# Optimization experiments

Hardware: AMD Instinct MI355X
Metric: run time of the kernel (lower is better)

## Reference

```python
import jax, jax.numpy as jnp
import numpy as np

DIM = 128
NUM_LAYERS = 2
FF_MULT = 4
RADIUS = 0.2
K = 8
B, N, L = 8, 2048, 4096
NEG = -1e30


def setup_inputs() -> dict:
    key = jax.random.key(0)
    ks = jax.random.split(key, 12)
    C = DIM
    s = 1.0 / np.sqrt(C)
    w = lambda k, shape, sc: jax.random.normal(k, shape, dtype=jnp.float32) * sc
    inp = {
        "q_xyz": jax.random.uniform(ks[0], (B, N, 3), dtype=jnp.float32),
        "q_feat": jax.random.normal(ks[1], (B, N, C), dtype=jnp.float32),
        "kv_xyz": jax.random.uniform(ks[2], (B, L, 3), dtype=jnp.float32),
        "kv_feat": jax.random.normal(ks[3], (B, L, C), dtype=jnp.float32),
        "kv_pad": jnp.zeros((B, L), dtype=bool),
        # PointTransformerConv params (stacked over layers)
        "W_lin": w(ks[4], (NUM_LAYERS, C, C), s),   # value projection (with bias)
        "b_lin": jnp.zeros((NUM_LAYERS, C), jnp.float32),
        "W_src": w(ks[5], (NUM_LAYERS, C, C), s),   # lin_src, no bias
        "W_dst": w(ks[6], (NUM_LAYERS, C, C), s),   # lin_dst, no bias
        "W_attn": w(ks[7], (NUM_LAYERS, C, C), s),  # attn_nn = Linear+ReLU
        "b_attn": jnp.zeros((NUM_LAYERS, C), jnp.float32),
        "ln1_g": jnp.ones((NUM_LAYERS, C), jnp.float32),
        "ln1_b": jnp.zeros((NUM_LAYERS, C), jnp.float32),
        "W_ff1": w(ks[8], (NUM_LAYERS, C, FF_MULT * C), s),
        "b_ff1": jnp.zeros((NUM_LAYERS, FF_MULT * C), jnp.float32),
        "W_ff2": w(ks[9], (NUM_LAYERS, FF_MULT * C, C), 1.0 / np.sqrt(FF_MULT * C)),
        "b_ff2": jnp.zeros((NUM_LAYERS, C), jnp.float32),
        "ln2_g": jnp.ones((NUM_LAYERS, C), jnp.float32),
        "ln2_b": jnp.zeros((NUM_LAYERS, C), jnp.float32),
    }
    return inp


def _layernorm(x, g, b):
    mu = x.mean(-1, keepdims=True)
    var = ((x - mu) ** 2).mean(-1, keepdims=True)
    return (x - mu) * jax.lax.rsqrt(var + 1e-5) * g + b


def _gather(feats, idx):
    # feats: [B, L, C], idx: [B, N, K] -> [B, N, K, C]
    b, n, k = idx.shape
    g = jnp.take_along_axis(feats, idx.reshape(b, n * k)[:, :, None], axis=1)
    return g.reshape(b, n, k, feats.shape[-1])


def _forward(q_xyz, q_feat, kv_xyz, kv_feat, kv_pad,
             W_lin, b_lin, W_src, W_dst, W_attn, b_attn,
             ln1_g, ln1_b, W_ff1, b_ff1, W_ff2, b_ff2, ln2_g, ln2_b):
    # radius neighbor search (per-batch, fixed K neighbors with validity mask)
    d2 = jnp.sum((q_xyz[:, :, None, :] - kv_xyz[:, None, :, :]) ** 2, axis=-1)  # [B,N,L]
    valid_pair = (d2 <= RADIUS * RADIUS) & (~kv_pad)[:, None, :]
    negd = jnp.where(valid_pair, -d2, NEG)
    negv, idx = jax.lax.top_k(negd, K)          # [B,N,K] nearest-in-ball
    evalid = negv > 0.5 * NEG                   # edge validity mask [B,N,K]

    out = q_feat
    for i in range(NUM_LAYERS):
        # PointTransformerConv, pos_nn = ZeroPos => delta = 0
        aj = _gather(kv_feat @ W_src[i], idx)                    # [B,N,K,C]
        vj = _gather(kv_feat @ W_lin[i] + b_lin[i], idx)         # [B,N,K,C]
        ai = out @ W_dst[i]                                      # [B,N,C]
        logits = jax.nn.relu((ai[:, :, None, :] - aj) @ W_attn[i] + b_attn[i])
        logits = jnp.where(evalid[..., None], logits, NEG)
        m = logits.max(axis=2, keepdims=True)
        e = jnp.exp(logits - m) * evalid[..., None]
        attn = e / jnp.maximum(e.sum(axis=2, keepdims=True), 1e-9)  # per-channel softmax over neighbors
        upd = jnp.sum(attn * vj, axis=2)                         # [B,N,C] scatter-add over edges
        out = _layernorm(out + upd, ln1_g[i], ln1_b[i])
        h = jax.nn.gelu(out @ W_ff1[i] + b_ff1[i], approximate=False)
        out = _layernorm(out + h @ W_ff2[i] + b_ff2[i], ln2_g[i], ln2_b[i])
    return out


def reference(q_xyz, q_feat, kv_xyz, kv_feat, kv_pad,
              W_lin, b_lin, W_src, W_dst, W_attn, b_attn,
              ln1_g, ln1_b, W_ff1, b_ff1, W_ff2, b_ff2, ln2_g, ln2_b):
    return _forward(q_xyz, q_feat, kv_xyz, kv_feat, kv_pad,
                    W_lin, b_lin, W_src, W_dst, W_attn, b_attn,
                    ln1_g, ln1_b, W_ff1, b_ff1, W_ff2, b_ff2, ln2_g, ln2_b)
```

## Files before the change

kernel.cpp:

```cpp
#include <hip/hip_runtime.h>
#include <hip/hip_bf16.h>
#include <math.h>

#define DIM 128
#define BB 8
#define NN 2048
#define LL 4096
#define KK 8

typedef __hip_bfloat16 bf16;
typedef unsigned long long ull;
typedef __attribute__((ext_vector_type(8))) short short8;
typedef __attribute__((ext_vector_type(4))) float float4v;

__device__ __forceinline__ float toF(float x){ return x; }
__device__ __forceinline__ float toF(bf16 x){ return __bfloat162float(x); }
__device__ __forceinline__ void st(float* p, float v){ *p = v; }
__device__ __forceinline__ void st(bf16*  p, float v){ *p = __float2bfloat16(v); }
__device__ __forceinline__ unsigned short f2bf(float f){
  union { bf16 b; unsigned short u; } cv; cv.b = __float2bfloat16(f); return cv.u;
}
__device__ __forceinline__ float2 ld2bf(const bf16* p){
  const unsigned u = *(const unsigned*)p;
  return make_float2(__uint_as_float(u << 16), __uint_as_float(u & 0xFFFF0000u));
}
__device__ __forceinline__ void st2bf(bf16* p, float a, float b){
  *(unsigned*)p = (unsigned)f2bf(a) | ((unsigned)f2bf(b) << 16);
}

__device__ __forceinline__ float gelu_exact(float x){
  return 0.5f * x * (1.0f + erff(x * 0.70710678118654752f));
}

__device__ __forceinline__ float waveSum64(float v){
  #pragma unroll
  for (int o = 32; o > 0; o >>= 1) v += __shfl_xor(v, o, 64);
  return v;
}
__device__ __forceinline__ float quadSum16(float v){
  #pragma unroll
  for (int o = 8; o > 0; o >>= 1) v += __shfl_xor(v, o, 64);
  return v;
}

__device__ __forceinline__ void topk_insert_u(ull (&m)[KK], ull key){
  m[KK-1] = key;
  #pragma unroll
  for (int t = KK-1; t > 0; --t){
    if (m[t] < m[t-1]){ ull tmp = m[t]; m[t] = m[t-1]; m[t-1] = tmp; }
  }
}

#define NC3 125
__device__ __forceinline__ void packOne(const float* __restrict__ src,
                                        bf16* __restrict__ dst, int idx, int nshift){
  const int k = idx >> nshift;
  const int n = idx & ((1 << nshift) - 1);
  const int N = 1 << nshift;
  st(&dst[((size_t)(k>>3)*N + n)*8 + (k&7)], src[idx]);
}

__global__ __launch_bounds__(1024) void setup_all(const float* __restrict__ kv_xyz,
                                                  const float* __restrict__ q_xyz,
                                                  float4* __restrict__ bpts,
                                                  int* __restrict__ offs,
                                                  int* __restrict__ qsrt,
                                                  const float* __restrict__ Wlin,
                                                  const float* __restrict__ Wff1,
                                                  const float* __restrict__ Wff2,
                                                  const float* __restrict__ Wsrc,
                                                  const float* __restrict__ Wdst,
                                                  const float* __restrict__ Wattn,
                                                  bf16* __restrict__ WlinP,
                                                  bf16* __restrict__ Wff1P,
                                                  bf16* __restrict__ Wff2P,
                                                  bf16* __restrict__ WsaP,
                                                  bf16* __restrict__ WdaP)
{
  __shared__ int cnt[NC3];
  __shared__ int off[NC3+1];
  __shared__ float row[8][DIM];
  const int bid = blockIdx.x;
  const int tid = threadIdx.x;
  if (bid < 16){
    const int b   = bid & 7;
    const int role= bid >> 3;
    if (tid < NC3) cnt[tid] = 0;
    __syncthreads();
    if (role == 0){
      const float* kvp = kv_xyz + (size_t)b * LL * 3;
      float px[4], py[4], pz[4]; int pc[4];
      #pragma unroll
      for (int i = 0; i < 4; i++){
        const int e = tid + i*1024;
        px[i] = kvp[3*e]; py[i] = kvp[3*e+1]; pz[i] = kvp[3*e+2];
        const int cx = min((int)(px[i]*5.f), 4);
        const int cy = min((int)(py[i]*5.f), 4);
        const int cz = min((int)(pz[i]*5.f), 4);
        pc[i] = (cz*5 + cy)*5 + cx;
        atomicAdd(&cnt[pc[i]], 1);
      }
      __syncthreads();
      if (tid == 0){
        int acc = 0;
        for (int c = 0; c < NC3; c++){ off[c] = acc; acc += cnt[c]; }
        off[NC3] = acc;
      }
      __syncthreads();
      if (tid < NC3) cnt[tid] = 0;
      __syncthreads();
      float4* dst = bpts + (size_t)b * LL;
      #pragma unroll
      for (int i = 0; i < 4; i++){
        const int e = tid + i*1024;
        const int pos = off[pc[i]] + atomicAdd(&cnt[pc[i]], 1);
        dst[pos] = make_float4(px[i], py[i], pz[i], __int_as_float(e));
      }
      if (tid < NC3 + 1) offs[b*126 + tid] = off[tid];
    } else {
      const float* qp = q_xyz + (size_t)b * NN * 3;
      int pc[2];
      #pragma unroll
      for (int i = 0; i < 2; i++){
        const int e = tid + i*1024;
        const float x = qp[3*e], y = qp[3*e+1], z = qp[3*e+2];
        const int cx = min((int)(x*5.f), 4);
        const int cy = min((int)(y*5.f), 4);
        const int cz = min((int)(z*5.f), 4);
        pc[i] = (cz*5 + cy)*5 + cx;
        atomicAdd(&cnt[pc[i]], 1);
      }
      __syncthreads();
      if (tid == 0){
        int acc = 0;
        for (int c = 0; c < NC3; c++){ off[c] = acc; acc += cnt[c]; }
        off[NC3] = acc;
      }
      __syncthreads();
      if (tid < NC3) cnt[tid] = 0;
      __syncthreads();
      int* dst = qsrt + (size_t)b * NN;
      #pragma unroll
      for (int i = 0; i < 2; i++){
        const int e = tid + i*1024;
        const int pos = off[pc[i]] + atomicAdd(&cnt[pc[i]], 1);
        dst[pos] = e;
      }
    }
  } else if (bid < 304){
    int i = (bid - 16)*1024 + tid;
    if (i < 32768){
      const int l = i >> 14, r = i & 16383;
      packOne(Wlin + (size_t)l*16384, WlinP + (size_t)l*16384, r, 7);
    } else if (i < 163840){
      i -= 32768;
      const int l = i >> 16, r = i & 65535;
      packOne(Wff1 + (size_t)l*65536, Wff1P + (size_t)l*65536, r, 9);
    } else {
      i -= 163840;
      const int l = i >> 16, r = i & 65535;
      packOne(Wff2 + (size_t)l*65536, Wff2P + (size_t)l*65536, r, 7);
    }
  } else {
    const int grp = tid >> 7;
    const int c = tid & 127;
    const int tt = (bid - 304)*8 + grp;
    const int r = tt & 127, which = (tt >> 7) & 1, lay = tt >> 8;
    const float* Wx = (which ? Wdst : Wsrc) + (size_t)lay*DIM*DIM;
    const float* Wa = Wattn + (size_t)lay*DIM*DIM;
    row[grp][c] = Wx[r*DIM + c];
    __syncthreads();
    float acc = 0.f;
    for (int j = 0; j < DIM; j++) acc = fmaf(row[grp][j], Wa[j*DIM + c], acc);
    bf16* dst = (which ? WdaP : WsaP) + (size_t)lay*DIM*DIM;
    st(&dst[((size_t)(r>>3)*DIM + c)*8 + (r&7)], acc);
  }
}

#define QBLK 8
#define SPL 32
__global__ __launch_bounds__(256) void knn_query(const float* __restrict__ q_xyz,
                                                 const float4* __restrict__ bpts,
                                                 const int* __restrict__ offs,
                                                 const int* __restrict__ qsrt,
                                                 int* __restrict__ idx)
{
  __shared__ ull cd[QBLK*257];
  const int tid  = threadIdx.x;
  const int s    = tid & 31;
  const int qloc = tid >> 5;
  const int b    = blockIdx.y;
  const int qbase = blockIdx.x * QBLK;
  const int qid = qsrt[b*NN + qbase + qloc];
  const size_t qo = ((size_t)b * NN + qid) * 3;
  const float qx = q_xyz[qo], qy = q_xyz[qo+1], qz = q_xyz[qo+2];
  const ull THRKEY = ((ull)0x3D23D70Bu << 32);
  ull kthr = THRKEY;
  ull m[KK];
  #pragma unroll
  for (int k = 0; k < KK; k++) m[k] = ~0ULL;
  const int qcx = min((int)(qx*5.f), 4);
  const int qcy = min((int)(qy*5.f), 4);
  const int qcz = min((int)(qz*5.f), 4);
  const int* ofb = offs + b*126;
  const float4* bp = bpts + (size_t)b * LL;
  const int cx0 = max(qcx-1, 0), cx1 = min(qcx+1, 4);
  int st9[9], en9[9];
  float4 hd[9];
  #pragma unroll
  for (int u = 0; u < 9; u++){
    const int dz = u/3 - 1, dy = u%3 - 1;
    const int cz = qcz + dz, cy = qcy + dy;
    const bool ok = (cz >= 0) & (cz <= 4) & (cy >= 0) & (cy <= 4);
    const int rowc = (cz*5 + cy)*5;
    int a0 = 0, e0 = 0;
    if (ok){ a0 = ofb[rowc + cx0] + s; e0 = ofb[rowc + cx1 + 1]; }
    st9[u] = a0; en9[u] = e0;
    const int pa = (a0 < e0) ? a0 : 0;
    hd[u] = bp[pa];
  }
  #pragma unroll
  for (int u = 0; u < 9; u++){
    int p = st9[u];
    const int e = en9[u];
    if (p < e){
      float4 pt = hd[u];
      while (true){
        const int pn = p + SPL;
        const bool hn = pn < e;
        float4 nx;
        if (hn) nx = bp[pn];
        const float dx = qx - pt.x, dy = qy - pt.y, dz = qz - pt.z;
        const float d2 = dx*dx + dy*dy + dz*dz;
        const ull key = ((ull)__float_as_uint(d2) << 32) | (unsigned)__float_as_int(pt.w);
        if (key < kthr){
          topk_insert_u(m, key);
          kthr = (m[KK-1] < THRKEY) ? m[KK-1] : THRKEY;
        }
        if (!hn) break;
        pt = nx; p = pn;
      }
    }
  }
  #pragma unroll
  for (int k = 0; k < KK; k++) cd[qloc*257 + k*32 + s] = m[k];
  __syncthreads();
  if (tid < 64){
    const int q = tid >> 3, g = tid & 7;
    ull mm[KK];
    #pragma unroll
    for (int k = 0; k < KK; k++) mm[k] = ~0ULL;
    #pragma unroll
    for (int u = 0; u < 4; u++){
      const int sl = g + 8*u;
      #pragma unroll
      for (int k = 0; k < KK; k++){
        const ull key = cd[q*257 + k*32 + sl];
        if (key < mm[KK-1]) topk_insert_u(mm, key);
      }
    }
    #pragma unroll
    for (int k = 0; k < KK; k++) cd[q*257 + k*32 + g] = mm[k];
    if (tid < QBLK){
      ull f[KK];
      #pragma unroll
      for (int k = 0; k < KK; k++) f[k] = ~0ULL;
      #pragma unroll
      for (int k = 0; k < 8; k++)
        for (int g2 = 0; g2 < 8; g2++){
          const ull key = cd[tid*257 + k*32 + g2];
          if (key < f[KK-1]) topk_insert_u(f, key);
        }
      const int oq = b * NN + qsrt[b*NN + qbase + tid];
      #pragma unroll
      for (int k = 0; k < KK; k++) idx[oq*KK + k] = (int)(unsigned)(f[k] & 0xFFFFFFFFu);
    }
  }
}

__device__ __forceinline__ void stage_A_f32(const float* __restrict__ A, size_t r0,
                                            int kd, int kc, unsigned short* As, int tid){
  #pragma unroll
  for (int i = 0; i < 8; i++){
    const int f = tid + i*256;
    const int row = f >> 5, c4 = (f & 31) * 4;
    const float4 v = *(const float4*)&A[(r0+row)*kd + kc + c4];
    uint2 u;
    u.x = (unsigned)f2bf(v.x) | ((unsigned)f2bf(v.y) << 16);
    u.y = (unsigned)f2bf(v.z) | ((unsigned)f2bf(v.w) << 16);
    *(uint2*)&As[row*136 + c4] = u;
  }
}
__device__ __forceinline__ void stage_A_bf16(const bf16* __restrict__ A, size_t r0,
                                             int kd, int kc, unsigned short* As, int tid){
  #pragma unroll
  for (int i = 0; i < 8; i++){
    const int f = tid + i*256;
    const int row = f >> 5, c4 = (f & 31) * 4;
    *(uint2*)&As[row*136 + c4] = *(const uint2*)&A[(r0+row)*kd + kc + c4];
  }
}

__global__ __launch_bounds__(256) void gemm_all(const float* __restrict__ kvf,
                                                const float* __restrict__ q_feat,
                                                const bf16* __restrict__ WsaP,
                                                const bf16* __restrict__ WlinP,
                                                const bf16* __restrict__ WdaP0,
                                                const float* __restrict__ b_lin,
                                                bf16* __restrict__ srcA0,
                                                bf16* __restrict__ linp0,
                                                bf16* __restrict__ srcA1,
                                                bf16* __restrict__ linp1,
                                                bf16* __restrict__ qA)
{
  __shared__ __align__(16) unsigned short As[64*136];
  const int bid = blockIdx.x;
  const int tid = threadIdx.x;
  const int wid = tid >> 6, ln = tid & 63, qd = ln >> 4, cl = ln & 15;
  if (bid < 1024){
    const int lay = bid >> 9;
    const size_t r0 = (size_t)(bid & 511) * 64;
    const bf16* Wp0 = WsaP  + (size_t)lay * DIM * DIM;
    const bf16* Wp1 = WlinP + (size_t)lay * DIM * DIM;
    const float* bias1 = b_lin + lay * DIM;
    bf16* Y0 = lay ? srcA1 : srcA0;
    bf16* Y1 = lay ? linp1 : linp0;
    stage_A_f32(kvf, r0, 128, 0, As, tid);
    __syncthreads();
    float4v ac0[8], ac1[8];
    #pragma unroll
    for (int t = 0; t < 8; t++){ ac0[t] = (float4v){0.f,0.f,0.f,0.f}; ac1[t] = (float4v){0.f,0.f,0.f,0.f}; }
    #pragma unroll
    for (int ks = 0; ks < 4; ks++){
      const short8 a = *(const short8*)&As[(wid*16 + cl)*136 + (ks*4 + qd)*8];
      const size_t wo = (size_t)(ks*4 + qd)*DIM + cl;
      const short8* wb0 = (const short8*)Wp0 + wo;
      const short8* wb1 = (const short8*)Wp1 + wo;
      #pragma unroll
      for (int t = 0; t < 8; t++){
        const short8 b0 = wb0[t*16];
        ac0[t] = __builtin_amdgcn_mfma_f32_16x16x32_bf16(a, b0, ac0[t], 0, 0, 0);
        const short8 b1 = wb1[t*16];
        ac1[t] = __builtin_amdgcn_mfma_f32_16x16x32_bf16(a, b1, ac1[t], 0, 0, 0);
      }
    }
    #pragma unroll
    for (int t = 0; t < 8; t++){
      const int col = t*16 + cl;
      const float bv = bias1[col];
      #pragma unroll
      for (int r = 0; r < 4; r++){
        const size_t row = r0 + wid*16 + qd*4 + r;
        st(&Y0[row*DIM + col], ac0[t][r]);
        st(&Y1[row*DIM + col], ac1[t][r] + bv);
      }
    }
  } else {
    const size_t r0 = (size_t)(bid - 1024) * 64;
    stage_A_f32(q_feat, r0, 128, 0, As, tid);
    __syncthreads();
    float4v acc[8];
    #pragma unroll
    for (int t = 0; t < 8; t++) acc[t] = (float4v){0.f,0.f,0.f,0.f};
    #pragma unroll
    for (int ks = 0; ks < 4; ks++){
      const short8 a = *(const short8*)&As[(wid*16 + cl)*136 + (ks*4 + qd)*8];
      const short8* wb = (const short8*)WdaP0 + (size_t)(ks*4 + qd)*DIM + cl;
      #pragma unroll
      for (int t = 0; t < 8; t++){
        const short8 b = wb[t*16];
        acc[t] = __builtin_amdgcn_mfma_f32_16x16x32_bf16(a, b, acc[t], 0, 0, 0);
      }
    }
    #pragma unroll
    for (int t = 0; t < 8; t++){
      const int col = t*16 + cl;
      #pragma unroll
      for (int r = 0; r < 4; r++){
        const size_t row = r0 + wid*16 + qd*4 + r;
        st(&qA[row*DIM + col], acc[t][r]);
      }
    }
  }
}

__global__ __launch_bounds__(256) void mfma_ff1(const bf16* __restrict__ A,
                                                const bf16* __restrict__ Wp,
                                                const float* __restrict__ bias,
                                                bf16* __restrict__ Y)
{
  __shared__ __align__(16) unsigned short As[64*136];
  const int tid = threadIdx.x;
  const size_t r0 = (size_t)blockIdx.x * 64;
  const int nblk = blockIdx.y * 128;
  stage_A_bf16(A, r0, 128, 0, As, tid);
  __syncthreads();
  const int wid = tid >> 6, ln = tid & 63, qd = ln >> 4, cl = ln & 15;
  float4v acc[8];
  #pragma unroll
  for (int t = 0; t < 8; t++) acc[t] = (float4v){0.f,0.f,0.f,0.f};
  #pragma unroll
  for (int ks = 0; ks < 4; ks++){
    const short8 a = *(const short8*)&As[(wid*16 + cl)*136 + (ks*4 + qd)*8];
    const short8* wb = (const short8*)Wp + (size_t)(ks*4 + qd)*512 + nblk + cl;
    #pragma unroll
    for (int t = 0; t < 8; t++){
      const short8 b = wb[t*16];
      acc[t] = __builtin_amdgcn_mfma_f32_16x16x32_bf16(a, b, acc[t], 0, 0, 0);
    }
  }
  #pragma unroll
  for (int t = 0; t < 8; t++){
    const int col = nblk + t*16 + cl;
    const float bv = bias[col];
    #pragma unroll
    for (int r = 0; r < 4; r++){
      const size_t row = r0 + wid*16 + qd*4 + r;
      st(&Y[row*512 + col], gelu_exact(acc[t][r] + bv));
    }
  }
}

template<bool EMITQA>
__global__ __launch_bounds__(256) void mfma_ff2ln(const bf16* __restrict__ A,
                                                  const bf16* __restrict__ Wp,
                                                  const float* __restrict__ b2,
                                                  const bf16* __restrict__ resid,
                                                  const float* __restrict__ g,
                                                  const float* __restrict__ bb,
                                                  float* __restrict__ Y,
                                                  const bf16* __restrict__ WqP,
                                                  bf16* __restrict__ qA)
{
  __shared__ __align__(16) unsigned short As[64*136];
  const int tid = threadIdx.x;
  const size_t r0 = (size_t)blockIdx.x * 64;
  const int wid = tid >> 6, ln = tid & 63, qd = ln >> 4, cl = ln & 15;
  float4v acc[8];
  #pragma unroll
  for (int t = 0; t < 8; t++) acc[t] = (float4v){0.f,0.f,0.f,0.f};
  for (int kc = 0; kc < 512; kc += 128){
    __syncthreads();
    stage_A_bf16(A, r0, 512, kc, As, tid);
    __syncthreads();
    const int k8c = kc >> 3;
    #pragma unroll
    for (int ks = 0; ks < 4; ks++){
      const short8 a = *(const short8*)&As[(wid*16 + cl)*136 + (ks*4 + qd)*8];
      const short8* wb = (const short8*)Wp + (size_t)(k8c + ks*4 + qd)*DIM + cl;
      #pragma unroll
      for (int t = 0; t < 8; t++){
        const short8 b = wb[t*16];
        acc[t] = __builtin_amdgcn_mfma_f32_16x16x32_bf16(a, b, acc[t], 0, 0, 0);
      }
    }
  }
  float v[8][4];
  #pragma unroll
  for (int t = 0; t < 8; t++){
    const int col = t*16 + cl;
    const float bv = b2[col];
    #pragma unroll
    for (int r = 0; r < 4; r++){
      const size_t row = r0 + wid*16 + qd*4 + r;
      v[t][r] = acc[t][r] + bv + toF(resid[row*DIM + col]);
    }
  }
  #pragma unroll
  for (int r = 0; r < 4; r++){
    float s = 0.f;
    #pragma unroll
    for (int t = 0; t < 8; t++) s += v[t][r];
    const float mu = quadSum16(s) * (1.f/DIM);
    float q = 0.f;
    #pragma unroll
    for (int t = 0; t < 8; t++){ const float d = v[t][r] - mu; q += d*d; }
    const float inv = rsqrtf(quadSum16(q) * (1.f/DIM) + 1e-5f);
    const size_t row = r0 + wid*16 + qd*4 + r;
    #pragma unroll
    for (int t = 0; t < 8; t++){
      const int col = t*16 + cl;
      const float y = (v[t][r] - mu) * inv * g[col] + bb[col];
      v[t][r] = y;
      Y[row*DIM + col] = y;
    }
  }
  if (EMITQA){
    __syncthreads();
    #pragma unroll
    for (int t = 0; t < 8; t++){
      #pragma unroll
      for (int r = 0; r < 4; r++)
        As[(wid*16 + qd*4 + r)*136 + t*16 + cl] = f2bf(v[t][r]);
    }
    float4v qacc[8];
    #pragma unroll
    for (int t = 0; t < 8; t++) qacc[t] = (float4v){0.f,0.f,0.f,0.f};
    #pragma unroll
    for (int ks = 0; ks < 4; ks++){
      const short8 a = *(const short8*)&As[(wid*16 + cl)*136 + (ks*4 + qd)*8];
      const short8* wb = (const short8*)WqP + (size_t)(ks*4 + qd)*DIM + cl;
      #pragma unroll
      for (int t = 0; t < 8; t++){
        const short8 b = wb[t*16];
        qacc[t] = __builtin_amdgcn_mfma_f32_16x16x32_bf16(a, b, qacc[t], 0, 0, 0);
      }
    }
    #pragma unroll
    for (int t = 0; t < 8; t++){
      const int col = t*16 + cl;
      #pragma unroll
      for (int r = 0; r < 4; r++){
        const size_t row = r0 + wid*16 + qd*4 + r;
        st(&qA[row*DIM + col], qacc[t][r]);
      }
    }
  }
}

__global__ __launch_bounds__(256) void attn_ln1(const bf16* __restrict__ qA,
                                                const bf16* __restrict__ srcA,
                                                const bf16* __restrict__ linp,
                                                const int* __restrict__ idx,
                                                const int* __restrict__ qsrt,
                                                const float* __restrict__ b_attn,
                                                const float* __restrict__ feat,
                                                const float* __restrict__ g,
                                                const float* __restrict__ bb,
                                                bf16* __restrict__ out1)
{
  const int tid = threadIdx.x;
  const int wv = tid >> 6, ln = tid & 63;
  const int sp = blockIdx.x * 4 + wv;
  const int b = sp >> 11;
  const int q = b * NN + qsrt[b*NN + (sp & 2047)];
  const bf16* sbase = srcA + (size_t)b * LL * DIM;
  const bf16* vbase = linp + (size_t)b * LL * DIM;
  const int c0 = 2*ln;
  const float2 ba = *(const float2*)&b_attn[c0];
  const float2 qa2 = ld2bf(&qA[(size_t)q*DIM + c0]);
  const float qa0 = qa2.x + ba.x, qa1 = qa2.y + ba.y;
  int ids[KK]; float l0[KK], l1[KK];
  float m0 = -1e30f, m1 = -1e30f;
  #pragma unroll
  for (int k = 0; k < KK; k++){
    const int id = idx[q*KK + k]; ids[k] = id;
    if (id >= 0){
      const float2 s2 = ld2bf(&sbase[(size_t)id*DIM + c0]);
      l0[k] = fmaxf(qa0 - s2.x, 0.f); m0 = fmaxf(m0, l0[k]);
      l1[k] = fmaxf(qa1 - s2.y, 0.f); m1 = fmaxf(m1, l1[k]);
    } else { l0[k] = 0.f; l1[k] = 0.f; }
  }
  float sum0 = 0.f, sum1 = 0.f, upd0 = 0.f, upd1 = 0.f;
  #pragma unroll
  for (int k = 0; k < KK; k++) if (ids[k] >= 0){
    const float e0 = expf(l0[k] - m0); l0[k] = e0; sum0 += e0;
    const float e1 = expf(l1[k] - m1); l1[k] = e1; sum1 += e1;
  }
  if (sum0 > 0.f){
    const float i0 = 1.f / sum0, i1 = 1.f / sum1;
    #pragma unroll
    for (int k = 0; k < KK; k++) if (ids[k] >= 0){
      const float2 v2 = ld2bf(&vbase[(size_t)ids[k]*DIM + c0]);
      upd0 = fmaf(l0[k]*i0, v2.x, upd0);
      upd1 = fmaf(l1[k]*i1, v2.y, upd1);
    }
  }
  const float2 f2 = *(const float2*)&feat[(size_t)q*DIM + c0];
  const float x0 = f2.x + upd0;
  const float x1 = f2.y + upd1;
  const float mu = waveSum64(x0 + x1) * (1.f/DIM);
  const float d0 = x0 - mu, d1 = x1 - mu;
  const float var = waveSum64(d0*d0 + d1*d1) * (1.f/DIM);
  const float inv = rsqrtf(var + 1e-5f);
  const float2 gg = *(const float2*)&g[c0];
  const float2 bbv = *(const float2*)&bb[c0];
  st2bf(&out1[(size_t)q*DIM + c0], d0 * inv * gg.x + bbv.x, d1 * inv * gg.y + bbv.y);
}

extern "C" void kernel_launch(void* const* d_in, const int* in_sizes, int n_in,
                              void* d_out, int out_size, void* d_ws, size_t ws_size,
                              hipStream_t stream)
{
  const float* q_xyz  = (const float*)d_in[0];
  const float* q_feat = (const float*)d_in[1];
  const float* kv_xyz = (const float*)d_in[2];
  const float* kv_feat= (const float*)d_in[3];
  const float* W_lin  = (const float*)d_in[5];
  const float* b_lin  = (const float*)d_in[6];
  const float* W_src  = (const float*)d_in[7];
  const float* W_dst  = (const float*)d_in[8];
  const float* W_attn = (const float*)d_in[9];
  const float* b_attn = (const float*)d_in[10];
  const float* ln1_g  = (const float*)d_in[11];
  const float* ln1_b  = (const float*)d_in[12];
  const float* W_ff1  = (const float*)d_in[13];
  const float* b_ff1  = (const float*)d_in[14];
  const float* W_ff2  = (const float*)d_in[15];
  const float* b_ff2  = (const float*)d_in[16];
  const float* ln2_g  = (const float*)d_in[17];
  const float* ln2_b  = (const float*)d_in[18];
  float* out = (float*)d_out;

  const int MQ  = BB * NN;
  const int MKV = BB * LL;

  char* p = (char*)d_ws;
  int*    idxb  = (int*)p;    p += (size_t)MQ * KK * 4;
  float4* bpts  = (float4*)p; p += (size_t)BB * LL * 16;
  int*    boffs = (int*)p;    p += (size_t)BB * 126 * 4;
  int*    qsrt  = (int*)p;    p += (size_t)BB * NN * 4;
  bf16*  WsaP  = (bf16*)p;  p += (size_t)2 * DIM * DIM * 2;
  bf16*  WdaP  = (bf16*)p;  p += (size_t)2 * DIM * DIM * 2;
  bf16*  WlinP = (bf16*)p;  p += (size_t)2 * DIM * DIM * 2;
  bf16*  Wff1P = (bf16*)p;  p += (size_t)2 * DIM * 4*DIM * 2;
  bf16*  Wff2P = (bf16*)p;  p += (size_t)2 * 4*DIM * DIM * 2;
  float* feat  = (float*)p; p += (size_t)MQ * DIM * 4;
  bf16*  out1  = (bf16*)p;  p += (size_t)MQ * DIM * 2;
  bf16*  srcA0 = (bf16*)p;  p += (size_t)MKV * DIM * 2;
  bf16*  linp0 = (bf16*)p;  p += (size_t)MKV * DIM * 2;
  bf16*  srcA1 = (bf16*)p;  p += (size_t)MKV * DIM * 2;
  bf16*  linp1 = (bf16*)p;  p += (size_t)MKV * DIM * 2;
  bf16*  qA    = (bf16*)p;  p += (size_t)MQ * DIM * 2;
  bf16*  hbuf  = (bf16*)p;  p += (size_t)MQ * 4*DIM * 2;

  setup_all<<<368, 1024, 0, stream>>>(kv_xyz, q_xyz, bpts, boffs, qsrt,
                                      W_lin, W_ff1, W_ff2, W_src, W_dst, W_attn,
                                      WlinP, Wff1P, Wff2P, WsaP, WdaP);
  knn_query<<<dim3(NN/QBLK, BB), 256, 0, stream>>>(q_xyz, bpts, boffs, qsrt, idxb);
  gemm_all<<<1280, 256, 0, stream>>>(kv_feat, q_feat, WsaP, WlinP, WdaP,
                                     b_lin, srcA0, linp0, srcA1, linp1, qA);

  attn_ln1<<<MQ/4, 256, 0, stream>>>(qA, srcA0, linp0, idxb, qsrt, b_attn,
                                     q_feat, ln1_g, ln1_b, out1);
  mfma_ff1<<<dim3(MQ/64, 4), 256, 0, stream>>>(out1, Wff1P, b_ff1, hbuf);
  mfma_ff2ln<true><<<MQ/64, 256, 0, stream>>>(hbuf, Wff2P, b_ff2, out1,
                                              ln2_g, ln2_b, feat,
                                              WdaP + DIM*DIM, qA);
  attn_ln1<<<MQ/4, 256, 0, stream>>>(qA, srcA1, linp1, idxb, qsrt, b_attn + DIM,
                                     feat, ln1_g + DIM, ln1_b + DIM, out1);
  mfma_ff1<<<dim3(MQ/64, 4), 256, 0, stream>>>(out1, Wff1P + DIM*4*DIM,
                                               b_ff1 + 4*DIM, hbuf);
  mfma_ff2ln<false><<<MQ/64, 256, 0, stream>>>(hbuf, Wff2P + 4*DIM*DIM,
                                               b_ff2 + DIM, out1,
                                               ln2_g + DIM, ln2_b + DIM, out,
                                               nullptr, nullptr);
}
```

Measured before the change: 284.8 us.

## Fuse FF1 and FF2+LN into one kernel and overlap weight packing with kNN

Fuses the FF1 GEMM with GELU into the FF2+LayerNorm kernel. Each 128-column hidden chunk is written to per-wave shared memory and consumed right away, so the MQ x 512 hidden buffer no longer round-trips through global memory. The residual is read from the staged shared A tile instead of global. Point binning is split into its own small kernel, and weight packing is interleaved with kNN query blocks in one launch so the packing work overlaps the search. Two launches per layer become one, at the cost of more shared memory per block and less FF1 parallelism, since there is no longer a grid dimension over N-blocks.

```diff
diff --git a/kernel.cpp b/kernel.cpp
--- a/kernel.cpp
+++ b/kernel.cpp
@@ -15,6 +15,9 @@
 
 __device__ __forceinline__ float toF(float x){ return x; }
 __device__ __forceinline__ float toF(bf16 x){ return __bfloat162float(x); }
+__device__ __forceinline__ float bfuToF(unsigned short u){
+  return __uint_as_float((unsigned)u << 16);
+}
 __device__ __forceinline__ void st(float* p, float v){ *p = v; }
 __device__ __forceinline__ void st(bf16*  p, float v){ *p = __float2bfloat16(v); }
 __device__ __forceinline__ unsigned short f2bf(float f){
@@ -52,6 +55,83 @@
 }
 
 #define NC3 125
+__global__ __launch_bounds__(1024) void bin_kernel(const float* __restrict__ kv_xyz,
+                                                   const float* __restrict__ q_xyz,
+                                                   float4* __restrict__ bpts,
+                                                   int* __restrict__ offs,
+                                                   int* __restrict__ qsrt)
+{
+  __shared__ int cnt[NC3];
+  __shared__ int off[NC3+1];
+  const int b   = blockIdx.x & 7;
+  const int role= blockIdx.x >> 3;
+  const int tid = threadIdx.x;
+  if (tid < NC3) cnt[tid] = 0;
+  __syncthreads();
+  if (role == 0){
+    const float* kvp = kv_xyz + (size_t)b * LL * 3;
+    float px[4], py[4], pz[4]; int pc[4];
+    #pragma unroll
+    for (int i = 0; i < 4; i++){
+      const int e = tid + i*1024;
+      px[i] = kvp[3*e]; py[i] = kvp[3*e+1]; pz[i] = kvp[3*e+2];
+      const int cx = min((int)(px[i]*5.f), 4);
+      const int cy = min((int)(py[i]*5.f), 4);
+      const int cz = min((int)(pz[i]*5.f), 4);
+      pc[i] = (cz*5 + cy)*5 + cx;
+      atomicAdd(&cnt[pc[i]], 1);
+    }
+    __syncthreads();
+    if (tid == 0){
+      int acc = 0;
+      for (int c = 0; c < NC3; c++){ off[c] = acc; acc += cnt[c]; }
+      off[NC3] = acc;
+    }
+    __syncthreads();
+    if (tid < NC3) cnt[tid] = 0;
+    __syncthreads();
+    float4* dst = bpts + (size_t)b * LL;
+    #pragma unroll
+    for (int i = 0; i < 4; i++){
+      const int e = tid + i*1024;
+      const int pos = off[pc[i]] + atomicAdd(&cnt[pc[i]], 1);
+      dst[pos] = make_float4(px[i], py[i], pz[i], __int_as_float(e));
+    }
+    if (tid < NC3 + 1) offs[b*126 + tid] = off[tid];
+  } else {
+    const float* qp = q_xyz + (size_t)b * NN * 3;
+    int pc[2];
+    #pragma unroll
+    for (int i = 0; i < 2; i++){
+      const int e = tid + i*1024;
+      const float x = qp[3*e], y = qp[3*e+1], z = qp[3*e+2];
+      const int cx = min((int)(x*5.f), 4);
+      const int cy = min((int)(y*5.f), 4);
+      const int cz = min((int)(z*5.f), 4);
+      pc[i] = (cz*5 + cy)*5 + cx;
+      atomicAdd(&cnt[pc[i]], 1);
+    }
+    __syncthreads();
+    if (tid == 0){
+      int acc = 0;
+      for (int c = 0; c < NC3; c++){ off[c] = acc; acc += cnt[c]; }
+      off[NC3] = acc;
+    }
+    __syncthreads();
+    if (tid < NC3) cnt[tid] = 0;
+    __syncthreads();
+    int* dst = qsrt + (size_t)b * NN;
+    #pragma unroll
+    for (int i = 0; i < 2; i++){
+      const int e = tid + i*1024;
+      const int pos = off[pc[i]] + atomicAdd(&cnt[pc[i]], 1);
+      dst[pos] = e;
+    }
+  }
+}
+
+#define QBLK 8
+#define SPL 32
 __device__ __forceinline__ void packOne(const float* __restrict__ src,
                                         bf16* __restrict__ dst, int idx, int nshift){
   const int k = idx >> nshift;
@@ -60,137 +140,67 @@
   st(&dst[((size_t)(k>>3)*N + n)*8 + (k&7)], src[idx]);
 }
 
-__global__ __launch_bounds__(1024) void setup_all(const float* __restrict__ kv_xyz,
-                                                  const float* __restrict__ q_xyz,
-                                                  float4* __restrict__ bpts,
-                                                  int* __restrict__ offs,
-                                                  int* __restrict__ qsrt,
-                                                  const float* __restrict__ Wlin,
-                                                  const float* __restrict__ Wff1,
-                                                  const float* __restrict__ Wff2,
-                                                  const float* __restrict__ Wsrc,
-                                                  const float* __restrict__ Wdst,
-                                                  const float* __restrict__ Wattn,
-                                                  bf16* __restrict__ WlinP,
-                                                  bf16* __restrict__ Wff1P,
-                                                  bf16* __restrict__ Wff2P,
-                                                  bf16* __restrict__ WsaP,
-                                                  bf16* __restrict__ WdaP)
+__global__ __launch_bounds__(256) void knn_pack(const float* __restrict__ q_xyz,
+                                                const float4* __restrict__ bpts,
+                                                const int* __restrict__ offs,
+                                                const int* __restrict__ qsrt,
+                                                int* __restrict__ idx,
+                                                const float* __restrict__ Wlin,
+                                                const float* __restrict__ Wff1,
+                                                const float* __restrict__ Wff2,
+                                                const float* __restrict__ Wsrc,
+                                                const float* __restrict__ Wdst,
+                                                const float* __restrict__ Wattn,
+                                                bf16* __restrict__ WlinP,
+                                                bf16* __restrict__ Wff1P,
+                                                bf16* __restrict__ Wff2P,
+                                                bf16* __restrict__ WsaP,
+                                                bf16* __restrict__ WdaP)
 {
-  __shared__ int cnt[NC3];
-  __shared__ int off[NC3+1];
-  __shared__ float row[8][DIM];
+  __shared__ __align__(16) unsigned char smem[16448];
   const int bid = blockIdx.x;
   const int tid = threadIdx.x;
-  if (bid < 16){
-    const int b   = bid & 7;
-    const int role= bid >> 3;
-    if (tid < NC3) cnt[tid] = 0;
-    __syncthreads();
-    if (role == 0){
-      const float* kvp = kv_xyz + (size_t)b * LL * 3;
-      float px[4], py[4], pz[4]; int pc[4];
-      #pragma unroll
-      for (int i = 0; i < 4; i++){
-        const int e = tid + i*1024;
-        px[i] = kvp[3*e]; py[i] = kvp[3*e+1]; pz[i] = kvp[3*e+2];
-        const int cx = min((int)(px[i]*5.f), 4);
-        const int cy = min((int)(py[i]*5.f), 4);
-        const int cz = min((int)(pz[i]*5.f), 4);
-        pc[i] = (cz*5 + cy)*5 + cx;
-        atomicAdd(&cnt[pc[i]], 1);
-      }
+  bool isKnn; int rid;
+  if (bid < 2816){ isKnn = !(bid & 1); rid = bid >> 1; }
+  else { isKnn = true; rid = 1408 + (bid - 2816); }
+
+  if (!isKnn){
+    if (rid < 1152){
+      int i = rid*256 + tid;
+      if (i < 32768){
+        const int l = i >> 14, r = i & 16383;
+        packOne(Wlin + (size_t)l*16384, WlinP + (size_t)l*16384, r, 7);
+      } else if (i < 163840){
+        i -= 32768;
+        const int l = i >> 16, r = i & 65535;
+        packOne(Wff1 + (size_t)l*65536, Wff1P + (size_t)l*65536, r, 9);
+      } else {
+        i -= 163840;
+        const int l = i >> 16, r = i & 65535;
+        packOne(Wff2 + (size_t)l*65536, Wff2P + (size_t)l*65536, r, 7);
+      }
+    } else {
+      float* row = (float*)smem;
+      const int half = tid >> 7;
+      const int c = tid & 127;
+      const int tt = (rid - 1152)*2 + half;
+      const int r = tt & 127, which = (tt >> 7) & 1, lay = tt >> 8;
+      const float* Wx = (which ? Wdst : Wsrc) + (size_t)lay*DIM*DIM;
+      const float* Wa = Wattn + (size_t)lay*DIM*DIM;
+      row[half*DIM + c] = Wx[r*DIM + c];
       __syncthreads();
-      if (tid == 0){
-        int acc = 0;
-        for (int c = 0; c < NC3; c++){ off[c] = acc; acc += cnt[c]; }
-        off[NC3] = acc;
-      }
-      __syncthreads();
-      if (tid < NC3) cnt[tid] = 0;
-      __syncthreads();
-      float4* dst = bpts + (size_t)b * LL;
-      #pragma unroll
-      for (int i = 0; i < 4; i++){
-        const int e = tid + i*1024;
-        const int pos = off[pc[i]] + atomicAdd(&cnt[pc[i]], 1);
-        dst[pos] = make_float4(px[i], py[i], pz[i], __int_as_float(e));
-      }
-      if (tid < NC3 + 1) offs[b*126 + tid] = off[tid];
-    } else {
-      const float* qp = q_xyz + (size_t)b * NN * 3;
-      int pc[2];
-      #pragma unroll
-      for (int i = 0; i < 2; i++){
-        const int e = tid + i*1024;
-        const float x = qp[3*e], y = qp[3*e+1], z = qp[3*e+2];
-        const int cx = min((int)(x*5.f), 4);
-        const int cy = min((int)(y*5.f), 4);
-        const int cz = min((int)(z*5.f), 4);
-        pc[i] = (cz*5 + cy)*5 + cx;
-        atomicAdd(&cnt[pc[i]], 1);
-      }
-      __syncthreads();
-      if (tid == 0){
-        int acc = 0;
-        for (int c = 0; c < NC3; c++){ off[c] = acc; acc += cnt[c]; }
-        off[NC3] = acc;
-      }
-      __syncthreads();
-      if (tid < NC3) cnt[tid] = 0;
-      __syncthreads();
-      int* dst = qsrt + (size_t)b * NN;
-      #pragma unroll
-      for (int i = 0; i < 2; i++){
-        const int e = tid + i*1024;
-        const int pos = off[pc[i]] + atomicAdd(&cnt[pc[i]], 1);
-        dst[pos] = e;
-      }
-    }
-  } else if (bid < 304){
-    int i = (bid - 16)*1024 + tid;
-    if (i < 32768){
-      const int l = i >> 14, r = i & 16383;
-      packOne(Wlin + (size_t)l*16384, WlinP + (size_t)l*16384, r, 7);
-    } else if (i < 163840){
-      i -= 32768;
-      const int l = i >> 16, r = i & 65535;
-      packOne(Wff1 + (size_t)l*65536, Wff1P + (size_t)l*65536, r, 9);
-    } else {
-      i -= 163840;
-      const int l = i >> 16, r = i & 65535;
-      packOne(Wff2 + (size_t)l*65536, Wff2P + (size_t)l*65536, r, 7);
-    }
-  } else {
-    const int grp = tid >> 7;
-    const int c = tid & 127;
-    const int tt = (bid - 304)*8 + grp;
-    const int r = tt & 127, which = (tt >> 7) & 1, lay = tt >> 8;
-    const float* Wx = (which ? Wdst : Wsrc) + (size_t)lay*DIM*DIM;
-    const float* Wa = Wattn + (size_t)lay*DIM*DIM;
-    row[grp][c] = Wx[r*DIM + c];
-    __syncthreads();
-    float acc = 0.f;
-    for (int j = 0; j < DIM; j++) acc = fmaf(row[grp][j], Wa[j*DIM + c], acc);
-    bf16* dst = (which ? WdaP : WsaP) + (size_t)lay*DIM*DIM;
-    st(&dst[((size_t)(r>>3)*DIM + c)*8 + (r&7)], acc);
-  }
-}
-
-#define QBLK 8
-#define SPL 32
-__global__ __launch_bounds__(256) void knn_query(const float* __restrict__ q_xyz,
-                                                 const float4* __restrict__ bpts,
-                                                 const int* __restrict__ offs,
-                                                 const int* __restrict__ qsrt,
-                                                 int* __restrict__ idx)
-{
-  __shared__ ull cd[QBLK*257];
-  const int tid  = threadIdx.x;
+      float acc = 0.f;
+      for (int j = 0; j < DIM; j++) acc = fmaf(row[half*DIM + j], Wa[j*DIM + c], acc);
+      bf16* dst = (which ? WdaP : WsaP) + (size_t)lay*DIM*DIM;
+      st(&dst[((size_t)(r>>3)*DIM + c)*8 + (r&7)], acc);
+    }
+    return;
+  }
+  ull* cd = (ull*)smem;
   const int s    = tid & 31;
   const int qloc = tid >> 5;
-  const int b    = blockIdx.y;
-  const int qbase = blockIdx.x * QBLK;
+  const int b    = rid >> 8;
+  const int qbase = (rid & 255) * QBLK;
   const int qid = qsrt[b*NN + qbase + qloc];
   const size_t qo = ((size_t)b * NN + qid) * 3;
   const float qx = q_xyz[qo], qy = q_xyz[qo+1], qz = q_xyz[qo+2];
@@ -384,74 +394,59 @@
   }
 }
 
-__global__ __launch_bounds__(256) void mfma_ff1(const bf16* __restrict__ A,
-                                                const bf16* __restrict__ Wp,
-                                                const float* __restrict__ bias,
-                                                bf16* __restrict__ Y)
+template<bool EMITQA>
+__global__ __launch_bounds__(256) void ff_fused(const bf16* __restrict__ A,
+                                                const bf16* __restrict__ W1p,
+                                                const float* __restrict__ b1,
+                                                const bf16* __restrict__ W2p,
+                                                const float* __restrict__ b2,
+                                                const float* __restrict__ g,
+                                                const float* __restrict__ bb,
+                                                float* __restrict__ Y,
+                                                const bf16* __restrict__ WqP,
+                                                bf16* __restrict__ qA)
 {
   __shared__ __align__(16) unsigned short As[64*136];
-  const int tid = threadIdx.x;
-  const size_t r0 = (size_t)blockIdx.x * 64;
-  const int nblk = blockIdx.y * 128;
-  stage_A_bf16(A, r0, 128, 0, As, tid);
-  __syncthreads();
-  const int wid = tid >> 6, ln = tid & 63, qd = ln >> 4, cl = ln & 15;
-  float4v acc[8];
-  #pragma unroll
-  for (int t = 0; t < 8; t++) acc[t] = (float4v){0.f,0.f,0.f,0.f};
-  #pragma unroll
-  for (int ks = 0; ks < 4; ks++){
-    const short8 a = *(const short8*)&As[(wid*16 + cl)*136 + (ks*4 + qd)*8];
-    const short8* wb = (const short8*)Wp + (size_t)(ks*4 + qd)*512 + nblk + cl;
-    #pragma unroll
-    for (int t = 0; t < 8; t++){
-      const short8 b = wb[t*16];
-      acc[t] = __builtin_amdgcn_mfma_f32_16x16x32_bf16(a, b, acc[t], 0, 0, 0);
-    }
-  }
-  #pragma unroll
-  for (int t = 0; t < 8; t++){
-    const int col = nblk + t*16 + cl;
-    const float bv = bias[col];
-    #pragma unroll
-    for (int r = 0; r < 4; r++){
-      const size_t row = r0 + wid*16 + qd*4 + r;
-      st(&Y[row*512 + col], gelu_exact(acc[t][r] + bv));
-    }
-  }
-}
-
-template<bool EMITQA>
-__global__ __launch_bounds__(256) void mfma_ff2ln(const bf16* __restrict__ A,
-                                                  const bf16* __restrict__ Wp,
-                                                  const float* __restrict__ b2,
-                                                  const bf16* __restrict__ resid,
-                                                  const float* __restrict__ g,
-                                                  const float* __restrict__ bb,
-                                                  float* __restrict__ Y,
-                                                  const bf16* __restrict__ WqP,
-                                                  bf16* __restrict__ qA)
-{
-  __shared__ __align__(16) unsigned short As[64*136];
+  __shared__ __align__(16) unsigned short Hs[4][16*136];
   const int tid = threadIdx.x;
   const size_t r0 = (size_t)blockIdx.x * 64;
   const int wid = tid >> 6, ln = tid & 63, qd = ln >> 4, cl = ln & 15;
-  float4v acc[8];
-  #pragma unroll
-  for (int t = 0; t < 8; t++) acc[t] = (float4v){0.f,0.f,0.f,0.f};
-  for (int kc = 0; kc < 512; kc += 128){
-    __syncthreads();
-    stage_A_bf16(A, r0, 512, kc, As, tid);
-    __syncthreads();
-    const int k8c = kc >> 3;
+  stage_A_bf16(A, r0, 128, 0, As, tid);
+  __syncthreads();
+  float4v acc2[8];
+  #pragma unroll
+  for (int t = 0; t < 8; t++) acc2[t] = (float4v){0.f,0.f,0.f,0.f};
+  #pragma unroll
+  for (int chunk = 0; chunk < 4; chunk++){
+    float4v h[8];
+    #pragma unroll
+    for (int t = 0; t < 8; t++) h[t] = (float4v){0.f,0.f,0.f,0.f};
     #pragma unroll
     for (int ks = 0; ks < 4; ks++){
       const short8 a = *(const short8*)&As[(wid*16 + cl)*136 + (ks*4 + qd)*8];
-      const short8* wb = (const short8*)Wp + (size_t)(k8c + ks*4 + qd)*DIM + cl;
+      const short8* wb = (const short8*)W1p + (size_t)(ks*4 + qd)*512 + chunk*128 + cl;
       #pragma unroll
       for (int t = 0; t < 8; t++){
         const short8 b = wb[t*16];
-        acc[t] = __builtin_amdgcn_mfma_f32_16x16x32_bf16(a, b, acc[t], 0, 0, 0);
+        h[t] = __builtin_amdgcn_mfma_f32_16x16x32_bf16(a, b, h[t], 0, 0, 0);
+      }
+    }
+    #pragma unroll
+    for (int t = 0; t < 8; t++){
+      const float bv = b1[chunk*128 + t*16 + cl];
+      #pragma unroll
+      for (int r = 0; r < 4; r++)
+        Hs[wid][(qd*4 + r)*136 + t*16 + cl] = f2bf(gelu_exact(h[t][r] + bv));
+    }
+    #pragma unroll
+    for (int ks = 0; ks < 4; ks++){
+      const short8 a2 = *(const short8*)&Hs[wid][cl*136 + (ks*4 + qd)*8];
+      const int k8 = chunk*16 + ks*4 + qd;
+      const short8* wb2 = (const short8*)W2p + (size_t)k8*DIM + cl;
+      #pragma unroll
+      for (int t = 0; t < 8; t++){
+        const short8 b = wb2[t*16];
+        acc2[t] = __builtin_amdgcn_mfma_f32_16x16x32_bf16(a2, b, acc2[t], 0, 0, 0);
       }
     }
   }
@@ -461,10 +456,8 @@
     const int col = t*16 + cl;
     const float bv = b2[col];
     #pragma unroll
-    for (int r = 0; r < 4; r++){
-      const size_t row = r0 + wid*16 + qd*4 + r;
-      v[t][r] = acc[t][r] + bv + toF(resid[row*DIM + col]);
-    }
+    for (int r = 0; r < 4; r++)
+      v[t][r] = acc2[t][r] + bv + bfuToF(As[(wid*16 + qd*4 + r)*136 + col]);
   }
   #pragma unroll
   for (int r = 0; r < 4; r++){
@@ -486,7 +479,6 @@
     }
   }
   if (EMITQA){
-    __syncthreads();
     #pragma unroll
     for (int t = 0; t < 8; t++){
       #pragma unroll
@@ -622,27 +614,23 @@
   bf16*  srcA1 = (bf16*)p;  p += (size_t)MKV * DIM * 2;
   bf16*  linp1 = (bf16*)p;  p += (size_t)MKV * DIM * 2;
   bf16*  qA    = (bf16*)p;  p += (size_t)MQ * DIM * 2;
-  bf16*  hbuf  = (bf16*)p;  p += (size_t)MQ * 4*DIM * 2;
-
-  setup_all<<<368, 1024, 0, stream>>>(kv_xyz, q_xyz, bpts, boffs, qsrt,
-                                      W_lin, W_ff1, W_ff2, W_src, W_dst, W_attn,
-                                      WlinP, Wff1P, Wff2P, WsaP, WdaP);
-  knn_query<<<dim3(NN/QBLK, BB), 256, 0, stream>>>(q_xyz, bpts, boffs, qsrt, idxb);
+
+  bin_kernel<<<16, 1024, 0, stream>>>(kv_xyz, q_xyz, bpts, boffs, qsrt);
+  knn_pack<<<3456, 256, 0, stream>>>(q_xyz, bpts, boffs, qsrt, idxb,
+                                     W_lin, W_ff1, W_ff2, W_src, W_dst, W_attn,
+                                     WlinP, Wff1P, Wff2P, WsaP, WdaP);
   gemm_all<<<1280, 256, 0, stream>>>(kv_feat, q_feat, WsaP, WlinP, WdaP,
                                      b_lin, srcA0, linp0, srcA1, linp1, qA);
 
   attn_ln1<<<MQ/4, 256, 0, stream>>>(qA, srcA0, linp0, idxb, qsrt, b_attn,
                                      q_feat, ln1_g, ln1_b, out1);
-  mfma_ff1<<<dim3(MQ/64, 4), 256, 0, stream>>>(out1, Wff1P, b_ff1, hbuf);
-  mfma_ff2ln<true><<<MQ/64, 256, 0, stream>>>(hbuf, Wff2P, b_ff2, out1,
-                                              ln2_g, ln2_b, feat,
-                                              WdaP + DIM*DIM, qA);
+  ff_fused<true><<<MQ/64, 256, 0, stream>>>(out1, Wff1P, b_ff1, Wff2P, b_ff2,
+                                            ln2_g, ln2_b, feat,
+                                            WdaP + DIM*DIM, qA);
   attn_ln1<<<MQ/4, 256, 0, stream>>>(qA, srcA1, linp1, idxb, qsrt, b_attn + DIM,
                                      feat, ln1_g + DIM, ln1_b + DIM, out1);
-  mfma_ff1<<<dim3(MQ/64, 4), 256, 0, stream>>>(out1, Wff1P + DIM*4*DIM,
-                                               b_ff1 + 4*DIM, hbuf);
-  mfma_ff2ln<false><<<MQ/64, 256, 0, stream>>>(hbuf, Wff2P + 4*DIM*DIM,
-                                               b_ff2 + DIM, out1,
-                                               ln2_g + DIM, ln2_b + DIM, out,
-                                               nullptr, nullptr);
-}
+  ff_fused<false><<<MQ/64, 256, 0, stream>>>(out1, Wff1P + DIM*4*DIM, b_ff1 + 4*DIM,
+                                             Wff2P + 4*DIM*DIM, b_ff2 + DIM,
+                                             ln2_g + DIM, ln2_b + DIM, out,
+                                             nullptr, nullptr);
+}
```

Result: slower. 391.7 us (+37.5%).
